# Performance work log

Hardware: AMD Instinct MI355X
Metric: run time of the kernel (lower is better)

The kernel has to match this reference:

```python
import jax, jax.numpy as jnp
import numpy as np

NUM_EXPERTS = 64
TOP_K = 2
MAX_SEQ_LENGTH = 4096
CAPACITY_FACTOR = 1.0
EXPERT_CAPACITY = int(CAPACITY_FACTOR * (MAX_SEQ_LENGTH * TOP_K) / NUM_EXPERTS)  # 128


def setup_inputs() -> dict:
    key = jax.random.key(0)
    k1, k2 = jax.random.split(key)
    hidden_states = jax.random.normal(k1, (8, 4096, 4096), dtype=jnp.float32)
    router_weight = jax.random.normal(k2, (NUM_EXPERTS, 4096), dtype=jnp.float32) * 0.02
    return {"hidden_states": hidden_states, "router_weight": router_weight}


def reference(hidden_states, router_weight):
    B, S, H = hidden_states.shape
    E, K, C = NUM_EXPERTS, TOP_K, EXPERT_CAPACITY

    # router projection + softmax
    router_logits = jnp.einsum('bsh,eh->bse', hidden_states, router_weight)
    router_probs = jax.nn.softmax(router_logits, axis=-1)

    # top-k experts per token, renormalized weights
    expert_weights, expert_indices = jax.lax.top_k(router_probs, K)  # [B,S,K]
    expert_weights = expert_weights / jnp.sum(expert_weights, axis=-1, keepdims=True)

    # Capacity-limited dispatch. The torch loops process slot k=0 for all tokens
    # (in seq order), then k=1, with a shared per-(batch,expert) counter that
    # saturates at capacity. Equivalent: order tokens k-major-then-seq, take an
    # exclusive cumsum of one-hot assignments, and keep entries with prior
    # attempt count < capacity.
    oh = jax.nn.one_hot(expert_indices, E, dtype=jnp.int32)        # [B,S,K,E]
    oh_ord = oh.transpose(0, 2, 1, 3).reshape(B, K * S, E)         # k-major ordering
    pos = jnp.cumsum(oh_ord, axis=1) - oh_ord                      # exclusive cumsum [B,KS,E]
    keep = ((pos < C) & (oh_ord == 1)).astype(hidden_states.dtype) # [B,KS,E]
    keep = keep.reshape(B, K, S, E)

    dispatch_tensor = jnp.sum(keep, axis=1)                                      # [B,S,E]
    combine_tensor = jnp.einsum('bkse,bsk->bse', keep, expert_weights)           # [B,S,E]

    aux_loss = jnp.mean(jnp.sum(router_probs * router_probs, axis=-1)) * E
    z_loss = jnp.mean(jax.scipy.special.logsumexp(router_logits, axis=-1) ** 2)
    return dispatch_tensor, combine_tensor, router_probs, aux_loss, z_loss
```

## Files before the change

### kernel.cpp

```cpp
#include <hip/hip_runtime.h>
#include <math.h>

#define NE 64
#define TPB 128
#define KC 64
#define HDIM 4096
#define SEQ 4096
#define NTOK 32768
#define CAP 128
#define LSTRIDE 65

__global__ __launch_bounds__(256) void k_router(
    const float* __restrict__ hs, const float* __restrict__ rw,
    float* __restrict__ dispatch, float* __restrict__ combine,
    float* __restrict__ probs_out,
    int* __restrict__ idx_buf, float* __restrict__ wgt_buf,
    float* __restrict__ partials)
{
    __shared__ double smemd[TPB * LSTRIDE];
    float* shh = (float*)smemd;
    float* sww = (float*)smemd + KC * TPB;
    double* sdl = smemd;
    __shared__ float red1[4], red2[4];

    const int tid = threadIdx.x;
    const int tokBase = blockIdx.x * TPB;

    const int eg = tid & 15;
    const int tg = tid >> 4;

    double acc[8][4];
#pragma unroll
    for (int i = 0; i < 8; ++i)
#pragma unroll
        for (int j = 0; j < 4; ++j) acc[i][j] = 0.0;

    const int t_ld = tid >> 1;
    const int kh_off = (tid & 1) * 32;
    const float* hrow = hs + (size_t)(tokBase + t_ld) * HDIM + kh_off;
    const int e_ld = tid >> 2;
    const int kw_off = (tid & 3) * 16;
    const float* wrow = rw + (size_t)e_ld * HDIM + kw_off;

    float4 hreg[8];
    float4 wreg[4];
#pragma unroll
    for (int i = 0; i < 8; ++i) hreg[i] = *(const float4*)(hrow + i * 4);
#pragma unroll
    for (int i = 0; i < 4; ++i) wreg[i] = *(const float4*)(wrow + i * 4);

    const int nChunks = HDIM / KC;
    for (int c = 0; c < nChunks; ++c) {
        __syncthreads();
#pragma unroll
        for (int i = 0; i < 8; ++i) {
            int kk = kh_off + i * 4;
            shh[(kk + 0) * TPB + t_ld] = hreg[i].x;
            shh[(kk + 1) * TPB + t_ld] = hreg[i].y;
            shh[(kk + 2) * TPB + t_ld] = hreg[i].z;
            shh[(kk + 3) * TPB + t_ld] = hreg[i].w;
        }
#pragma unroll
        for (int i = 0; i < 4; ++i) {
            int kk = kw_off + i * 4;
            sww[(kk + 0) * NE + e_ld] = wreg[i].x;
            sww[(kk + 1) * NE + e_ld] = wreg[i].y;
            sww[(kk + 2) * NE + e_ld] = wreg[i].z;
            sww[(kk + 3) * NE + e_ld] = wreg[i].w;
        }
        __syncthreads();
        if (c + 1 < nChunks) {
            const float* hp = hrow + (size_t)(c + 1) * KC;
#pragma unroll
            for (int i = 0; i < 8; ++i) hreg[i] = *(const float4*)(hp + i * 4);
            const float* wp = wrow + (size_t)(c + 1) * KC;
#pragma unroll
            for (int i = 0; i < 4; ++i) wreg[i] = *(const float4*)(wp + i * 4);
        }
#pragma unroll 2
        for (int k = 0; k < KC; ++k) {
            float4 w  = *(const float4*)&sww[k * NE + 4 * eg];
            float4 h0 = *(const float4*)&shh[k * TPB + 8 * tg];
            float4 h1 = *(const float4*)&shh[k * TPB + 8 * tg + 4];
            double hd[8] = {(double)h0.x, (double)h0.y, (double)h0.z, (double)h0.w,
                            (double)h1.x, (double)h1.y, (double)h1.z, (double)h1.w};
            double wd[4] = {(double)w.x, (double)w.y, (double)w.z, (double)w.w};
#pragma unroll
            for (int i = 0; i < 8; ++i)
#pragma unroll
                for (int j = 0; j < 4; ++j)
                    acc[i][j] = fma(hd[i], wd[j], acc[i][j]);
        }
    }

    __syncthreads();
#pragma unroll
    for (int i = 0; i < 8; ++i)
#pragma unroll
        for (int j = 0; j < 4; ++j)
            sdl[(size_t)(8 * tg + i) * LSTRIDE + 4 * eg + j] = acc[i][j];
    __syncthreads();

    {
        float4 z4 = make_float4(0.f, 0.f, 0.f, 0.f);
        float4* dp = (float4*)(dispatch + (size_t)tokBase * NE);
        float4* cp = (float4*)(combine + (size_t)tokBase * NE);
#pragma unroll
        for (int m = 0; m < 8; ++m) {
            dp[m * 256 + tid] = z4;
            cp[m * 256 + tid] = z4;
        }
    }

    float p2 = 0.f, zl = 0.f;
    if (tid < TPB) {
        const int t = tid;
        const double* rowd = &sdl[(size_t)t * LSTRIDE];

        double mx = -1.0e300;
        double b0 = -1.0e300, b1 = -1.0e300;
        int i0 = 0, i1 = 0;
        for (int e = 0; e < NE; ++e) {
            double l = rowd[e];
            mx = fmax(mx, l);
            if (l > b0)      { b1 = b0; i1 = i0; b0 = l; i0 = e; }
            else if (l > b1) { b1 = l; i1 = e; }
        }

        float fp[NE];
        double sum = 0.0;
#pragma unroll
        for (int e = 0; e < NE; ++e) {
            double ds = exp(rowd[e] - mx);
            sum += ds;
            fp[e] = (float)ds;
        }
        float sumf = (float)sum;

        float p2l = 0.f;
#pragma unroll
        for (int e = 0; e < NE; ++e) {
            float p = fp[e] / sumf;
            fp[e] = p;
            p2l += p * p;
        }
        float4* gp = (float4*)(probs_out + (size_t)(tokBase + t) * NE);
#pragma unroll
        for (int q = 0; q < 16; ++q) gp[q] = *(float4*)&fp[4 * q];

        p2 = p2l;
        double lse = mx + log(sum);
        zl = (float)(lse * lse);

        double w0 = 1.0 / (1.0 + exp(b1 - b0));
        double w1 = 1.0 / (1.0 + exp(b0 - b1));
        idx_buf[(size_t)(tokBase + t) * 2 + 0] = i0;
        idx_buf[(size_t)(tokBase + t) * 2 + 1] = i1;
        wgt_buf[(size_t)(tokBase + t) * 2 + 0] = (float)w0;
        wgt_buf[(size_t)(tokBase + t) * 2 + 1] = (float)w1;
    }

#pragma unroll
    for (int off = 32; off; off >>= 1) {
        p2 += __shfl_down(p2, off);
        zl += __shfl_down(zl, off);
    }
    const int lane = tid & 63, wid = tid >> 6;
    if (lane == 0) { red1[wid] = p2; red2[wid] = zl; }
    __syncthreads();
    if (tid == 0) {
        partials[blockIdx.x * 2 + 0] = red1[0] + red1[1] + red1[2] + red1[3];
        partials[blockIdx.x * 2 + 1] = red2[0] + red2[1] + red2[2] + red2[3];
    }
}

__global__ __launch_bounds__(256) void k_dispatch(
    const int* __restrict__ idx_buf, const float* __restrict__ wgt_buf,
    float* __restrict__ dispatch, float* __restrict__ combine)
{
    const int e = blockIdx.x & 63;
    const int b = blockIdx.x >> 6;
    __shared__ int wc[4];
    const int tid = threadIdx.x;
    const int lane = tid & 63, wid = tid >> 6;
    const int base = b * SEQ;

    int running = 0;
    for (int chunk = 0; chunk < 32; ++chunk) {
        int j = chunk * 256 + tid;
        int k = j >> 12;
        int s = j & (SEQ - 1);
        int my = idx_buf[(size_t)(base + s) * 2 + k];
        bool m = (my == e);
        unsigned long long bal = __ballot(m);
        int prefix = __popcll(bal & ((1ull << lane) - 1ull));
        if (lane == 0) wc[wid] = __popcll(bal);
        __syncthreads();
        int woff = 0, tot = 0;
#pragma unroll
        for (int w = 0; w < 4; ++w) {
            int c = wc[w];
            tot += c;
            if (w < wid) woff += c;
        }
        if (m) {
            int pos = running + woff + prefix;
            if (pos < CAP) {
                size_t o = (size_t)(base + s) * NE + e;
                dispatch[o] = 1.0f;
                combine[o] = wgt_buf[(size_t)(base + s) * 2 + k];
            }
        }
        running += tot;
        __syncthreads();
    }
}

__global__ __launch_bounds__(256) void k_final(
    const float* __restrict__ partials, float* __restrict__ out)
{
    __shared__ float r1[4], r2[4];
    const int tid = threadIdx.x;
    float a = partials[tid * 2 + 0];
    float b = partials[tid * 2 + 1];
#pragma unroll
    for (int off = 32; off; off >>= 1) {
        a += __shfl_down(a, off);
        b += __shfl_down(b, off);
    }
    const int lane = tid & 63, wid = tid >> 6;
    if (lane == 0) { r1[wid] = a; r2[wid] = b; }
    __syncthreads();
    if (tid == 0) {
        float at = r1[0] + r1[1] + r1[2] + r1[3];
        float bt = r2[0] + r2[1] + r2[2] + r2[3];
        out[0] = at / (float)NTOK * (float)NE;
        out[1] = bt / (float)NTOK;
    }
}

extern "C" void kernel_launch(void* const* d_in, const int* in_sizes, int n_in,
                              void* d_out, int out_size, void* d_ws, size_t ws_size,
                              hipStream_t stream)
{
    const float* hs = (const float*)d_in[0];
    const float* rw = (const float*)d_in[1];
    float* out = (float*)d_out;
    float* dispatch = out;
    float* combine  = out + 2097152;
    float* probs    = out + 2 * 2097152;
    float* scalars  = out + 3 * 2097152;

    int*   idx_buf  = (int*)d_ws;
    float* wgt_buf  = (float*)((char*)d_ws + 65536 * 4);
    float* partials = (float*)((char*)d_ws + 65536 * 8);

    hipLaunchKernelGGL(k_router, dim3(NTOK / TPB), dim3(256), 0, stream,
                       hs, rw, dispatch, combine, probs, idx_buf, wgt_buf, partials);
    hipLaunchKernelGGL(k_dispatch, dim3(8 * NE), dim3(256), 0, stream,
                       idx_buf, wgt_buf, dispatch, combine);
    hipLaunchKernelGGL(k_final, dim3(1), dim3(256), 0, stream,
                       partials, scalars);
}
```

Before: 1.085 ms.

## Compute router logits in fp32 with fp64 recompute for ambiguous top-k tokens

Replaces the fp64 FMA router matmul with an fp32 4x4 register-tiled GEMM over 64-token tiles, and does the softmax in fp32. Tokens whose top-3 logit gaps fall below a threshold are appended to a list with an atomic counter, and a new fixup kernel recomputes their logits in fp64 to settle expert selection and weights. This removes the costly double-precision inner loop. The risk is that the heuristic threshold may miss near-tie cases, and the atomic list adds a small serial cost.

```diff
diff --git a/kernel.cpp b/kernel.cpp
--- a/kernel.cpp
+++ b/kernel.cpp
@@ -2,25 +2,25 @@
 #include <math.h>
 
 #define NE 64
-#define TPB 128
+#define TPB 64
 #define KC 64
 #define HDIM 4096
 #define SEQ 4096
 #define NTOK 32768
 #define CAP 128
-#define LSTRIDE 65
+#define LS 68
+#define AMB_TH 2.0e-3f
 
 __global__ __launch_bounds__(256) void k_router(
     const float* __restrict__ hs, const float* __restrict__ rw,
     float* __restrict__ dispatch, float* __restrict__ combine,
     float* __restrict__ probs_out,
     int* __restrict__ idx_buf, float* __restrict__ wgt_buf,
-    float* __restrict__ partials)
-{
-    __shared__ double smemd[TPB * LSTRIDE];
-    float* shh = (float*)smemd;
-    float* sww = (float*)smemd + KC * TPB;
-    double* sdl = smemd;
+    float* __restrict__ partials,
+    int* __restrict__ fix_cnt, int* __restrict__ fix_list)
+{
+    __shared__ float shh[KC * LS];
+    __shared__ float sww[KC * LS];
     __shared__ float red1[4], red2[4];
 
     const int tid = threadIdx.x;
@@ -29,23 +29,20 @@
     const int eg = tid & 15;
     const int tg = tid >> 4;
 
-    double acc[8][4];
-#pragma unroll
-    for (int i = 0; i < 8; ++i)
-#pragma unroll
-        for (int j = 0; j < 4; ++j) acc[i][j] = 0.0;
-
-    const int t_ld = tid >> 1;
-    const int kh_off = (tid & 1) * 32;
-    const float* hrow = hs + (size_t)(tokBase + t_ld) * HDIM + kh_off;
-    const int e_ld = tid >> 2;
-    const int kw_off = (tid & 3) * 16;
-    const float* wrow = rw + (size_t)e_ld * HDIM + kw_off;
-
-    float4 hreg[8];
-    float4 wreg[4];
-#pragma unroll
-    for (int i = 0; i < 8; ++i) hreg[i] = *(const float4*)(hrow + i * 4);
+    float acc[4][4];
+#pragma unroll
+    for (int i = 0; i < 4; ++i)
+#pragma unroll
+        for (int j = 0; j < 4; ++j) acc[i][j] = 0.f;
+
+    const int r_ld  = tid & 63;
+    const int k_off = (tid >> 6) * 16;
+    const float* hrow = hs + (size_t)(tokBase + r_ld) * HDIM + k_off;
+    const float* wrow = rw + (size_t)r_ld * HDIM + k_off;
+
+    float4 hreg[4], wreg[4];
+#pragma unroll
+    for (int i = 0; i < 4; ++i) hreg[i] = *(const float4*)(hrow + i * 4);
 #pragma unroll
     for (int i = 0; i < 4; ++i) wreg[i] = *(const float4*)(wrow + i * 4);
 
@@ -53,60 +50,54 @@
     for (int c = 0; c < nChunks; ++c) {
         __syncthreads();
 #pragma unroll
-        for (int i = 0; i < 8; ++i) {
-            int kk = kh_off + i * 4;
-            shh[(kk + 0) * TPB + t_ld] = hreg[i].x;
-            shh[(kk + 1) * TPB + t_ld] = hreg[i].y;
-            shh[(kk + 2) * TPB + t_ld] = hreg[i].z;
-            shh[(kk + 3) * TPB + t_ld] = hreg[i].w;
-        }
-#pragma unroll
         for (int i = 0; i < 4; ++i) {
-            int kk = kw_off + i * 4;
-            sww[(kk + 0) * NE + e_ld] = wreg[i].x;
-            sww[(kk + 1) * NE + e_ld] = wreg[i].y;
-            sww[(kk + 2) * NE + e_ld] = wreg[i].z;
-            sww[(kk + 3) * NE + e_ld] = wreg[i].w;
+            const int kk = k_off + i * 4;
+            shh[(kk + 0) * LS + r_ld] = hreg[i].x;
+            shh[(kk + 1) * LS + r_ld] = hreg[i].y;
+            shh[(kk + 2) * LS + r_ld] = hreg[i].z;
+            shh[(kk + 3) * LS + r_ld] = hreg[i].w;
+            sww[(kk + 0) * LS + r_ld] = wreg[i].x;
+            sww[(kk + 1) * LS + r_ld] = wreg[i].y;
+            sww[(kk + 2) * LS + r_ld] = wreg[i].z;
+            sww[(kk + 3) * LS + r_ld] = wreg[i].w;
         }
         __syncthreads();
         if (c + 1 < nChunks) {
             const float* hp = hrow + (size_t)(c + 1) * KC;
-#pragma unroll
-            for (int i = 0; i < 8; ++i) hreg[i] = *(const float4*)(hp + i * 4);
             const float* wp = wrow + (size_t)(c + 1) * KC;
 #pragma unroll
+            for (int i = 0; i < 4; ++i) hreg[i] = *(const float4*)(hp + i * 4);
+#pragma unroll
             for (int i = 0; i < 4; ++i) wreg[i] = *(const float4*)(wp + i * 4);
         }
-#pragma unroll 2
+#pragma unroll 8
         for (int k = 0; k < KC; ++k) {
-            float4 w  = *(const float4*)&sww[k * NE + 4 * eg];
-            float4 h0 = *(const float4*)&shh[k * TPB + 8 * tg];
-            float4 h1 = *(const float4*)&shh[k * TPB + 8 * tg + 4];
-            double hd[8] = {(double)h0.x, (double)h0.y, (double)h0.z, (double)h0.w,
-                            (double)h1.x, (double)h1.y, (double)h1.z, (double)h1.w};
-            double wd[4] = {(double)w.x, (double)w.y, (double)w.z, (double)w.w};
-#pragma unroll
-            for (int i = 0; i < 8; ++i)
+            const float4 h = *(const float4*)&shh[k * LS + 4 * tg];
+            const float4 w = *(const float4*)&sww[k * LS + 4 * eg];
+            const float hv[4] = {h.x, h.y, h.z, h.w};
+            const float wv[4] = {w.x, w.y, w.z, w.w};
+#pragma unroll
+            for (int i = 0; i < 4; ++i)
 #pragma unroll
                 for (int j = 0; j < 4; ++j)
-                    acc[i][j] = fma(hd[i], wd[j], acc[i][j]);
+                    acc[i][j] = fmaf(hv[i], wv[j], acc[i][j]);
         }
     }
 
     __syncthreads();
 #pragma unroll
-    for (int i = 0; i < 8; ++i)
+    for (int i = 0; i < 4; ++i)
 #pragma unroll
         for (int j = 0; j < 4; ++j)
-            sdl[(size_t)(8 * tg + i) * LSTRIDE + 4 * eg + j] = acc[i][j];
+            shh[(4 * tg + i) * LS + 4 * eg + j] = acc[i][j];
     __syncthreads();
 
     {
-        float4 z4 = make_float4(0.f, 0.f, 0.f, 0.f);
+        const float4 z4 = make_float4(0.f, 0.f, 0.f, 0.f);
         float4* dp = (float4*)(dispatch + (size_t)tokBase * NE);
         float4* cp = (float4*)(combine + (size_t)tokBase * NE);
 #pragma unroll
-        for (int m = 0; m < 8; ++m) {
+        for (int m = 0; m < 4; ++m) {
             dp[m * 256 + tid] = z4;
             cp[m * 256 + tid] = z4;
         }
@@ -114,50 +105,53 @@
 
     float p2 = 0.f, zl = 0.f;
     if (tid < TPB) {
-        const int t = tid;
-        const double* rowd = &sdl[(size_t)t * LSTRIDE];
-
-        double mx = -1.0e300;
-        double b0 = -1.0e300, b1 = -1.0e300;
+        const float* rowl = &shh[tid * LS];
+
+        float b0 = -3.4e38f, b1 = -3.4e38f, b2 = -3.4e38f;
         int i0 = 0, i1 = 0;
+#pragma unroll
         for (int e = 0; e < NE; ++e) {
-            double l = rowd[e];
-            mx = fmax(mx, l);
-            if (l > b0)      { b1 = b0; i1 = i0; b0 = l; i0 = e; }
-            else if (l > b1) { b1 = l; i1 = e; }
+            const float l = rowl[e];
+            if (l > b0)      { b2 = b1; b1 = b0; i1 = i0; b0 = l; i0 = e; }
+            else if (l > b1) { b2 = b1; b1 = l; i1 = e; }
+            else if (l > b2) { b2 = l; }
         }
 
         float fp[NE];
-        double sum = 0.0;
+        float sum = 0.f;
 #pragma unroll
         for (int e = 0; e < NE; ++e) {
-            double ds = exp(rowd[e] - mx);
-            sum += ds;
-            fp[e] = (float)ds;
-        }
-        float sumf = (float)sum;
-
+            const float s = expf(rowl[e] - b0);
+            sum += s;
+            fp[e] = s;
+        }
+        const float inv = 1.f / sum;
         float p2l = 0.f;
 #pragma unroll
         for (int e = 0; e < NE; ++e) {
-            float p = fp[e] / sumf;
+            const float p = fp[e] * inv;
             fp[e] = p;
             p2l += p * p;
         }
-        float4* gp = (float4*)(probs_out + (size_t)(tokBase + t) * NE);
+        float4* gp = (float4*)(probs_out + (size_t)(tokBase + tid) * NE);
 #pragma unroll
         for (int q = 0; q < 16; ++q) gp[q] = *(float4*)&fp[4 * q];
 
         p2 = p2l;
-        double lse = mx + log(sum);
-        zl = (float)(lse * lse);
-
-        double w0 = 1.0 / (1.0 + exp(b1 - b0));
-        double w1 = 1.0 / (1.0 + exp(b0 - b1));
-        idx_buf[(size_t)(tokBase + t) * 2 + 0] = i0;
-        idx_buf[(size_t)(tokBase + t) * 2 + 1] = i1;
-        wgt_buf[(size_t)(tokBase + t) * 2 + 0] = (float)w0;
-        wgt_buf[(size_t)(tokBase + t) * 2 + 1] = (float)w1;
+        const float lse = b0 + logf(sum);
+        zl = lse * lse;
+
+        const float w0 = 1.f / (1.f + expf(b1 - b0));
+        const float w1 = 1.f / (1.f + expf(b0 - b1));
+        idx_buf[(size_t)(tokBase + tid) * 2 + 0] = i0;
+        idx_buf[(size_t)(tokBase + tid) * 2 + 1] = i1;
+        wgt_buf[(size_t)(tokBase + tid) * 2 + 0] = w0;
+        wgt_buf[(size_t)(tokBase + tid) * 2 + 1] = w1;
+
+        if ((b0 - b1 < AMB_TH) || (b1 - b2 < AMB_TH)) {
+            const int p = atomicAdd(fix_cnt, 1);
+            fix_list[p] = tokBase + tid;
+        }
     }
 
 #pragma unroll
@@ -171,6 +165,56 @@
     if (tid == 0) {
         partials[blockIdx.x * 2 + 0] = red1[0] + red1[1] + red1[2] + red1[3];
         partials[blockIdx.x * 2 + 1] = red2[0] + red2[1] + red2[2] + red2[3];
+    }
+}
+
+__global__ __launch_bounds__(256) void k_fixup(
+    const float* __restrict__ hs, const float* __restrict__ rw,
+    const int* __restrict__ fix_cnt, const int* __restrict__ fix_list,
+    int* __restrict__ idx_buf, float* __restrict__ wgt_buf)
+{
+    __shared__ double part[NE][5];
+    __shared__ double lg[NE];
+    const int tid = threadIdx.x;
+    const int e  = tid & 63;
+    const int kq = tid >> 6;
+    const int n = fix_cnt[0];
+
+    for (int fi = blockIdx.x; fi < n; fi += gridDim.x) {
+        const int t = fix_list[fi];
+        const float4* hp = (const float4*)(hs + (size_t)t * HDIM + kq * 1024);
+        const float4* wp = (const float4*)(rw + (size_t)e * HDIM + kq * 1024);
+        double a = 0.0;
+#pragma unroll 4
+        for (int i = 0; i < 256; ++i) {
+            const float4 h = hp[i];
+            const float4 w = wp[i];
+            a = fma((double)h.x, (double)w.x, a);
+            a = fma((double)h.y, (double)w.y, a);
+            a = fma((double)h.z, (double)w.z, a);
+            a = fma((double)h.w, (double)w.w, a);
+        }
+        part[e][kq] = a;
+        __syncthreads();
+        if (tid < NE)
+            lg[tid] = part[tid][0] + part[tid][1] + part[tid][2] + part[tid][3];
+        __syncthreads();
+        if (tid == 0) {
+            double b0 = -1.0e300, b1 = -1.0e300;
+            int i0 = 0, i1 = 0;
+            for (int x = 0; x < NE; ++x) {
+                const double l = lg[x];
+                if (l > b0)      { b1 = b0; i1 = i0; b0 = l; i0 = x; }
+                else if (l > b1) { b1 = l; i1 = x; }
+            }
+            const double w0 = 1.0 / (1.0 + exp(b1 - b0));
+            const double w1 = 1.0 / (1.0 + exp(b0 - b1));
+            idx_buf[(size_t)t * 2 + 0] = i0;
+            idx_buf[(size_t)t * 2 + 1] = i1;
+            wgt_buf[(size_t)t * 2 + 0] = (float)w0;
+            wgt_buf[(size_t)t * 2 + 1] = (float)w1;
+        }
+        __syncthreads();
     }
 }
 
@@ -221,8 +265,8 @@
 {
     __shared__ float r1[4], r2[4];
     const int tid = threadIdx.x;
-    float a = partials[tid * 2 + 0];
-    float b = partials[tid * 2 + 1];
+    float a = partials[tid * 2 + 0] + partials[(tid + 256) * 2 + 0];
+    float b = partials[tid * 2 + 1] + partials[(tid + 256) * 2 + 1];
 #pragma unroll
     for (int off = 32; off; off >>= 1) {
         a += __shfl_down(a, off);
@@ -254,9 +298,15 @@
     int*   idx_buf  = (int*)d_ws;
     float* wgt_buf  = (float*)((char*)d_ws + 65536 * 4);
     float* partials = (float*)((char*)d_ws + 65536 * 8);
-
+    int*   fix_cnt  = (int*)((char*)d_ws + 65536 * 8 + 4096);
+    int*   fix_list = (int*)((char*)d_ws + 65536 * 8 + 8192);
+
+    hipMemsetAsync(fix_cnt, 0, sizeof(int), stream);
     hipLaunchKernelGGL(k_router, dim3(NTOK / TPB), dim3(256), 0, stream,
-                       hs, rw, dispatch, combine, probs, idx_buf, wgt_buf, partials);
+                       hs, rw, dispatch, combine, probs, idx_buf, wgt_buf,
+                       partials, fix_cnt, fix_list);
+    hipLaunchKernelGGL(k_fixup, dim3(256), dim3(256), 0, stream,
+                       hs, rw, fix_cnt, fix_list, idx_buf, wgt_buf);
     hipLaunchKernelGGL(k_dispatch, dim3(8 * NE), dim3(256), 0, stream,
                        idx_buf, wgt_buf, dispatch, combine);
     hipLaunchKernelGGL(k_final, dim3(1), dim3(256), 0, stream,
```

Measured after the change: 951.5 us. 12.3% less time.
